# Kernel tuning notes

Measured on AMD Instinct MI355X. Metric: run time of the kernel, lower is better.

## Reference

```python
import jax, jax.numpy as jnp
import numpy as np

HEADS = 8
TOPK = 32
LN_EPS = 1e-5


def _ln(x, g, b):
    m = jnp.mean(x, axis=-1, keepdims=True)
    v = jnp.var(x, axis=-1, keepdims=True)
    return (x - m) * jax.lax.rsqrt(v + LN_EPS) * g + b


def _split_heads(t):
    B, N, I = t.shape
    return t.reshape(B, N, HEADS, I // HEADS).transpose(0, 2, 1, 3)


def _merge_heads(t):
    B, H, N, D = t.shape
    return t.transpose(0, 2, 1, 3).reshape(B, N, H * D)


def _mha(xq, xkv, wq, wk, wv, wo, bo):
    # standard softmax cross-attention (SDPA branch, topk<=0), scale=1/sqrt(d_head)
    q = _split_heads(xq @ wq)
    k = _split_heads(xkv @ wk)
    v = _split_heads(xkv @ wv)
    scale = q.shape[-1] ** -0.5
    attn = jax.nn.softmax(jnp.einsum('bhnd,bhmd->bhnm', q, k) * scale, axis=-1)
    o = jnp.einsum('bhnm,bhmd->bhnd', attn, v)
    return _merge_heads(o) @ wo + bo


def _topk_attn(x, wq, wk, wv, wo, bo):
    # top-k sparse self-attention branch: softmax over the k largest logits per query,
    # all other attention weights are exactly zero -> equivalent to gathering the
    # selected value rows and contracting (avoids materializing the scattered matrix).
    q = _split_heads(x @ wq)
    k = _split_heads(x @ wk)
    v = _split_heads(x @ wv)
    scale = q.shape[-1] ** -0.5
    dots = jnp.einsum('bhnd,bhmd->bhnm', q, k) * scale  # [B,H,N,N]
    top_dots, top_inds = jax.lax.top_k(dots, TOPK)      # [B,H,N,K]
    top_attn = jax.nn.softmax(top_dots, axis=-1)
    # v_sel[b,h,n,k,d] = v[b,h,top_inds[b,h,n,k],d]
    v_sel = jnp.take_along_axis(v[:, :, None, :, :], top_inds[..., None], axis=3)
    o = jnp.einsum('bhnk,bhnkd->bhnd', top_attn, v_sel)
    return _merge_heads(o) @ wo + bo


def _geglu_ff(x, w1, b1, w2, b2):
    h = x @ w1 + b1
    a, g = jnp.split(h, 2, axis=-1)
    return (a * jax.nn.gelu(g, approximate=False)) @ w2 + b2


def _forward(x, context,
             ctx_wq, ctx_wk, ctx_wv, ctx_wo, ctx_bo, cn_g, cn_b,
             im_wq, im_wk, im_wv, im_wo, im_bo,
             xc_wq, xc_wk, xc_wv, xc_wo, xc_bo,
             ffc_w1, ffc_b1, ffc_w2, ffc_b2,
             ffi_w1, ffi_b1, ffi_w2, ffi_b2,
             n1_g, n1_b, n2_g, n2_b, n3_g, n3_b):
    # context self-attention (nx_enhanced=1) + context feed-forward
    cn = _ln(context, cn_g, cn_b)
    c = context + _mha(cn, cn, ctx_wq, ctx_wk, ctx_wv, ctx_wo, ctx_bo)
    c = c + _geglu_ff(c, ffc_w1, ffc_b1, ffc_w2, ffc_b2)
    # image-token top-k sparse self-attention
    h = x + _topk_attn(_ln(x, n1_g, n1_b), im_wq, im_wk, im_wv, im_wo, im_bo)
    # image -> context cross-attention
    h = h + _mha(_ln(h, n2_g, n2_b), c, xc_wq, xc_wk, xc_wv, xc_wo, xc_bo)
    # image feed-forward (GEGLU)
    h = h + _geglu_ff(_ln(h, n3_g, n3_b), ffi_w1, ffi_b1, ffi_w2, ffi_b2)
    return h


def setup_inputs() -> dict:
    key = jax.random.key(0)
    ki = iter(jax.random.split(key, 64))
    def w(*shape):
        return jax.random.normal(next(ki), shape, jnp.float32) * 0.02
    C, D, I = 768, 512, 512
    inp = dict(
        x=jax.random.normal(next(ki), (2, 2304, D), jnp.float32),
        context=jax.random.normal(next(ki), (2, 256, C), jnp.float32),
        spatial_shapes=jnp.array([[48, 48]], dtype=jnp.int32),  # 48*48 == 2304
        ctx_wq=w(C, I), ctx_wk=w(C, I), ctx_wv=w(C, I), ctx_wo=w(I, C),
        ctx_bo=jnp.zeros((C,), jnp.float32),
        cn_g=jnp.ones((C,), jnp.float32), cn_b=jnp.zeros((C,), jnp.float32),
        im_wq=w(D, I), im_wk=w(D, I), im_wv=w(D, I), im_wo=w(I, D),
        im_bo=jnp.zeros((D,), jnp.float32),
        xc_wq=w(D, I), xc_wk=w(C, I), xc_wv=w(C, I), xc_wo=w(I, D),
        xc_bo=jnp.zeros((D,), jnp.float32),
        ffc_w1=w(C, 8 * C), ffc_b1=jnp.zeros((8 * C,), jnp.float32),
        ffc_w2=w(4 * C, C), ffc_b2=jnp.zeros((C,), jnp.float32),
        ffi_w1=w(D, 8 * D), ffi_b1=jnp.zeros((8 * D,), jnp.float32),
        ffi_w2=w(4 * D, D), ffi_b2=jnp.zeros((D,), jnp.float32),
        n1_g=jnp.ones((D,), jnp.float32), n1_b=jnp.zeros((D,), jnp.float32),
        n2_g=jnp.ones((D,), jnp.float32), n2_b=jnp.zeros((D,), jnp.float32),
        n3_g=jnp.ones((D,), jnp.float32), n3_b=jnp.zeros((D,), jnp.float32),
    )
    return inp


def reference(x, context, spatial_shapes,
              ctx_wq, ctx_wk, ctx_wv, ctx_wo, ctx_bo, cn_g, cn_b,
              im_wq, im_wk, im_wv, im_wo, im_bo,
              xc_wq, xc_wk, xc_wv, xc_wo, xc_bo,
              ffc_w1, ffc_b1, ffc_w2, ffc_b2,
              ffi_w1, ffi_b1, ffi_w2, ffi_b2,
              n1_g, n1_b, n2_g, n2_b, n3_g, n3_b):
    del spatial_shapes  # only consumed by the (disabled) deformable path
    return _forward(x, context,
                    ctx_wq, ctx_wk, ctx_wv, ctx_wo, ctx_bo, cn_g, cn_b,
                    im_wq, im_wk, im_wv, im_wo, im_bo,
                    xc_wq, xc_wk, xc_wv, xc_wo, xc_bo,
                    ffc_w1, ffc_b1, ffc_w2, ffc_b2,
                    ffi_w1, ffi_b1, ffi_w2, ffi_b2,
                    n1_g, n1_b, n2_g, n2_b, n3_g, n3_b)
```

## Files before the change

### kernel.cpp

```cpp
#include <hip/hip_runtime.h>
#include <hip/hip_bf16.h>
#include <hip/hip_fp16.h>
#include <cmath>

typedef unsigned short u16;
typedef unsigned long long ull;
typedef __attribute__((ext_vector_type(8))) short short8;
typedef __attribute__((ext_vector_type(4))) float f32x4;
typedef __attribute__((ext_vector_type(4))) unsigned short u16x4;

__device__ __forceinline__ u16 f2bf(float x) {
    unsigned u = __float_as_uint(x);
    u += 0x7fffu + ((u >> 16) & 1u);
    return (u16)(u >> 16);
}
__device__ __forceinline__ float bf2f(u16 b) {
    return __uint_as_float(((unsigned)b) << 16);
}

__device__ __forceinline__ unsigned h2key(unsigned hb) {
    return (hb & 0x8000u) ? (hb ^ 0xFFFFu) : (hb | 0x8000u);
}
__device__ __forceinline__ float key2f(unsigned k) {
    unsigned hb = (k & 0x8000u) ? (k ^ 0x8000u) : (k ^ 0xFFFFu);
    return __half2float(__ushort_as_half((unsigned short)hb));
}

typedef __attribute__((address_space(3))) unsigned int as3_uint;
typedef __attribute__((address_space(1))) unsigned int as1_uint;
__device__ __forceinline__ void gload_lds16(const u16* g, u16* l) {
    __builtin_amdgcn_global_load_lds(
        (as1_uint*)(unsigned long long)(const void*)g,
        (as3_uint*)(unsigned int)(unsigned long long)(const void*)l,
        16, 0, 0);
}

__device__ __forceinline__ float gelu_exact(float g) {
    return 0.5f * g * (1.f + erff(g * 0.70710678118654752f));
}

struct TBatch {
    const float* src[16];
    u16* dst[16];
    int K[16];
    int N[16];
    int start[17];
};

__global__ void k_transpose_cast_batch(TBatch tb) {
    __shared__ float tile[32][33];
    int t = blockIdx.x;
    int m = 0;
    while (t >= tb.start[m + 1]) ++m;
    int rel = t - tb.start[m];
    const int K = tb.K[m], N = tb.N[m];
    const int ntx = N >> 5;
    const int n0 = (rel % ntx) * 32, k0 = (rel / ntx) * 32;
    const float* __restrict__ in = tb.src[m];
    u16* __restrict__ out = tb.dst[m];
    int tx = threadIdx.x, ty = threadIdx.y;
#pragma unroll
    for (int j = 0; j < 4; ++j)
        tile[ty + j * 8][tx] = in[(size_t)(k0 + ty + j * 8) * N + n0 + tx];
    __syncthreads();
#pragma unroll
    for (int j = 0; j < 4; ++j)
        out[(size_t)(n0 + ty + j * 8) * K + k0 + tx] = f2bf(tile[tx][ty + j * 8]);
}

__global__ void k_vtrans16(const u16* __restrict__ in, int stride, int coloff,
                           u16* __restrict__ out) {
    __shared__ int tile[32][33];
    int tx = threadIdx.x, ty = threadIdx.y;
    int d0 = blockIdx.x * 32, k0 = blockIdx.y * 32, b = blockIdx.z;
#pragma unroll
    for (int j = 0; j < 4; ++j)
        tile[ty + j * 8][tx] = in[(size_t)(b * 256 + k0 + ty + j * 8) * stride + coloff + d0 + tx];
    __syncthreads();
#pragma unroll
    for (int j = 0; j < 4; ++j)
        out[(size_t)(b * 512 + d0 + ty + j * 8) * 256 + k0 + tx] = (u16)tile[tx][ty + j * 8];
}

__global__ __launch_bounds__(256)
void k_ln_bf16(const float* __restrict__ in, const float* __restrict__ gam,
               const float* __restrict__ bet, u16* __restrict__ out, int F) {
    int lane = threadIdx.x & 63, w = threadIdx.x >> 6;
    int row = blockIdx.x * 4 + w;
    const int F4 = F >> 2;
    const float4* r4 = reinterpret_cast<const float4*>(in + (size_t)row * F);
    const float4* g4 = reinterpret_cast<const float4*>(gam);
    const float4* b4 = reinterpret_cast<const float4*>(bet);
    float s = 0.f, s2 = 0.f;
    for (int j = lane; j < F4; j += 64) {
        float4 v = r4[j];
        s += v.x + v.y + v.z + v.w;
        s2 += v.x * v.x + v.y * v.y + v.z * v.z + v.w * v.w;
    }
#pragma unroll
    for (int off = 32; off; off >>= 1) { s += __shfl_xor(s, off); s2 += __shfl_xor(s2, off); }
    float mean = s / F;
    float var  = s2 / F - mean * mean;
    float inv  = 1.f / sqrtf(var + 1e-5f);
    u16x4* o4 = reinterpret_cast<u16x4*>(out + (size_t)row * F);
    for (int j = lane; j < F4; j += 64) {
        float4 v = r4[j], gm = g4[j], bt = b4[j];
        u16x4 o;
        o[0] = f2bf((v.x - mean) * inv * gm.x + bt.x);
        o[1] = f2bf((v.y - mean) * inv * gm.y + bt.y);
        o[2] = f2bf((v.z - mean) * inv * gm.z + bt.z);
        o[3] = f2bf((v.w - mean) * inv * gm.w + bt.w);
        o4[j] = o;
    }
}

template <int BM, int BN>
__global__ __launch_bounds__(256)
void gemm_bt(const u16* __restrict__ A, const u16* __restrict__ Bt,
             const float* __restrict__ bias, const float* __restrict__ res,
             float* __restrict__ out32, u16* __restrict__ out16,
             int M, int N, int K) {
    constexpr int WM = BM / 2, WN = BN / 2, FM = WM / 16, FN = WN / 16;
    __shared__ __align__(16) u16 As[BM * 32];
    __shared__ __align__(16) u16 Bs[BN * 32];
    const int tid = threadIdx.x;
    const int lane = tid & 63;
    const int wid = tid >> 6;
    const int wr = wid >> 1, wc = wid & 1;
    const int nwg = gridDim.x * gridDim.y;
    int lin = blockIdx.y * gridDim.x + blockIdx.x;
    lin = (lin & 7) * (nwg >> 3) + (lin >> 3);
    const int m0 = (lin / gridDim.x) * BM, n0 = (lin % gridDim.x) * BN;
    const int r16 = lane & 15;
    const int g8  = (lane >> 4) * 8;
    const int w16 = wid * 16;
    const int ln4 = lane >> 2;
    const int cb8 = (lane & 3) * 8;

    const f32x4 zero4 = {0.f, 0.f, 0.f, 0.f};
    f32x4 acc[FM][FN];
#pragma unroll
    for (int m = 0; m < FM; ++m)
#pragma unroll
        for (int n = 0; n < FN; ++n) acc[m][n] = zero4;

    for (int k0 = 0; k0 < K; k0 += 32) {
#pragma unroll
        for (int p = 0; p < BM / 64; ++p) {
            const int rb = p * 64 + w16;
            gload_lds16(A + (size_t)(m0 + rb + ln4) * K + k0 + cb8, &As[rb * 32]);
        }
#pragma unroll
        for (int p = 0; p < BN / 64; ++p) {
            const int rb = p * 64 + w16;
            gload_lds16(Bt + (size_t)(n0 + rb + ln4) * K + k0 + cb8, &Bs[rb * 32]);
        }
        __syncthreads();
        short8 af[FM], bfr[FN];
#pragma unroll
        for (int m = 0; m < FM; ++m)
            af[m] = *reinterpret_cast<const short8*>(&As[(wr * WM + m * 16 + r16) * 32 + g8]);
#pragma unroll
        for (int n = 0; n < FN; ++n)
            bfr[n] = *reinterpret_cast<const short8*>(&Bs[(wc * WN + n * 16 + r16) * 32 + g8]);
#pragma unroll
        for (int m = 0; m < FM; ++m)
#pragma unroll
            for (int n = 0; n < FN; ++n)
                acc[m][n] = __builtin_amdgcn_mfma_f32_16x16x32_bf16(af[m], bfr[n], acc[m][n], 0, 0, 0);
        __syncthreads();
    }

    const int rg = (lane >> 4) * 4;
#pragma unroll
    for (int m = 0; m < FM; ++m) {
#pragma unroll
        for (int n = 0; n < FN; ++n) {
#pragma unroll
            for (int j = 0; j < 4; ++j) {
                int row = m0 + wr * WM + m * 16 + rg + j;
                int col = n0 + wc * WN + n * 16 + r16;
                float v = acc[m][n][j];
                if (bias) v += bias[col];
                size_t off = (size_t)row * N + col;
                if (res) v += res[off];
                if (out32) out32[off] = v;
                if (out16) out16[off] = f2bf(v);
            }
        }
    }
}

template <int BM>
__global__ __launch_bounds__(256)
void gemm_geglu(const u16* __restrict__ A, const u16* __restrict__ Bt,
                const float* __restrict__ bias, u16* __restrict__ out16,
                int M, int Nh, int K) {
    constexpr int WM = BM / 2, FM = WM / 16;
    __shared__ __align__(16) u16 As[BM * 32];
    __shared__ __align__(16) u16 Bs[128 * 32];
    const int tid = threadIdx.x;
    const int lane = tid & 63;
    const int wid = tid >> 6;
    const int wr = wid >> 1, wc = wid & 1;
    const int nwg = gridDim.x * gridDim.y;
    int lin = blockIdx.y * gridDim.x + blockIdx.x;
    lin = (lin & 7) * (nwg >> 3) + (lin >> 3);
    const int m0 = (lin / gridDim.x) * BM, n0 = (lin % gridDim.x) * 64;
    const int r16 = lane & 15;
    const int g8  = (lane >> 4) * 8;
    const int w16 = wid * 16;
    const int ln4 = lane >> 2;
    const int cb8 = (lane & 3) * 8;

    const f32x4 zero4 = {0.f, 0.f, 0.f, 0.f};
    f32x4 acc_a[FM][2], acc_g[FM][2];
#pragma unroll
    for (int m = 0; m < FM; ++m)
#pragma unroll
        for (int n = 0; n < 2; ++n) { acc_a[m][n] = zero4; acc_g[m][n] = zero4; }

    for (int k0 = 0; k0 < K; k0 += 32) {
#pragma unroll
        for (int p = 0; p < BM / 64; ++p) {
            const int rb = p * 64 + w16;
            gload_lds16(A + (size_t)(m0 + rb + ln4) * K + k0 + cb8, &As[rb * 32]);
        }
        gload_lds16(Bt + (size_t)(n0 + w16 + ln4) * K + k0 + cb8, &Bs[w16 * 32]);
        gload_lds16(Bt + (size_t)(Nh + n0 + w16 + ln4) * K + k0 + cb8, &Bs[(64 + w16) * 32]);
        __syncthreads();
        short8 af[FM], ba[2], bg[2];
#pragma unroll
        for (int m = 0; m < FM; ++m)
            af[m] = *reinterpret_cast<const short8*>(&As[(wr * WM + m * 16 + r16) * 32 + g8]);
#pragma unroll
        for (int n = 0; n < 2; ++n) {
            ba[n] = *reinterpret_cast<const short8*>(&Bs[(wc * 32 + n * 16 + r16) * 32 + g8]);
            bg[n] = *reinterpret_cast<const short8*>(&Bs[(64 + wc * 32 + n * 16 + r16) * 32 + g8]);
        }
#pragma unroll
        for (int m = 0; m < FM; ++m)
#pragma unroll
            for (int n = 0; n < 2; ++n) {
                acc_a[m][n] = __builtin_amdgcn_mfma_f32_16x16x32_bf16(af[m], ba[n], acc_a[m][n], 0, 0, 0);
                acc_g[m][n] = __builtin_amdgcn_mfma_f32_16x16x32_bf16(af[m], bg[n], acc_g[m][n], 0, 0, 0);
            }
        __syncthreads();
    }

    const int rg = (lane >> 4) * 4;
#pragma unroll
    for (int m = 0; m < FM; ++m) {
#pragma unroll
        for (int n = 0; n < 2; ++n) {
#pragma unroll
            for (int j = 0; j < 4; ++j) {
                int row = m0 + wr * WM + m * 16 + rg + j;
                int col = n0 + wc * 32 + n * 16 + r16;
                float a = acc_a[m][n][j] + bias[col];
                float g = acc_g[m][n][j] + bias[Nh + col];
                out16[(size_t)row * Nh + col] = f2bf(a * gelu_exact(g));
            }
        }
    }
}

__global__ __launch_bounds__(256)
void k_attn_mfma(const u16* __restrict__ Qb, int sq, const u16* __restrict__ Kb,
                 int sk, const u16* __restrict__ VT, u16* __restrict__ out, int NQ) {
    __shared__ float sc[16][268];
    __shared__ u16   pb[16][268];
    const int tid = threadIdx.x, lane = tid & 63, w = tid >> 6;
    const int nqb = NQ >> 4;
    const int h = blockIdx.x & 7;
    const int rest = blockIdx.x >> 3;
    const int b = rest / nqb;
    const int q0 = (rest % nqb) << 4;
    const int r16 = lane & 15, g8 = (lane >> 4) * 8, rq = (lane >> 4) * 4;

    const size_t qrow = ((size_t)(b * NQ + q0 + r16)) * sq + h * 64;
    const short8 af0 = *reinterpret_cast<const short8*>(Qb + qrow + g8);
    const short8 af1 = *reinterpret_cast<const short8*>(Qb + qrow + 32 + g8);
    const u16* kb = Kb + (size_t)b * 256 * sk + h * 64;
    const f32x4 zero4 = {0.f, 0.f, 0.f, 0.f};
#pragma unroll
    for (int t = 0; t < 4; ++t) {
        const size_t krow = (size_t)(t * 64 + w * 16 + r16) * sk;
        const short8 bf0 = *reinterpret_cast<const short8*>(kb + krow + g8);
        const short8 bf1 = *reinterpret_cast<const short8*>(kb + krow + 32 + g8);
        f32x4 acc = __builtin_amdgcn_mfma_f32_16x16x32_bf16(af0, bf0, zero4, 0, 0, 0);
        acc = __builtin_amdgcn_mfma_f32_16x16x32_bf16(af1, bf1, acc, 0, 0, 0);
        const int col = t * 64 + w * 16 + r16;
#pragma unroll
        for (int j = 0; j < 4; ++j) sc[rq + j][col] = acc[j] * 0.125f;
    }
    __syncthreads();
#pragma unroll
    for (int qi = 0; qi < 4; ++qi) {
        const int q = w * 4 + qi;
        float4 v = *reinterpret_cast<const float4*>(&sc[q][lane * 4]);
        float m = fmaxf(fmaxf(v.x, v.y), fmaxf(v.z, v.w));
#pragma unroll
        for (int off = 32; off; off >>= 1) m = fmaxf(m, __shfl_xor(m, off));
        float e0 = expf(v.x - m), e1 = expf(v.y - m), e2 = expf(v.z - m), e3 = expf(v.w - m);
        float sum = e0 + e1 + e2 + e3;
#pragma unroll
        for (int off = 32; off; off >>= 1) sum += __shfl_xor(sum, off);
        float inv = 1.f / sum;
        u16x4 p4;
        p4[0] = f2bf(e0 * inv); p4[1] = f2bf(e1 * inv);
        p4[2] = f2bf(e2 * inv); p4[3] = f2bf(e3 * inv);
        *reinterpret_cast<u16x4*>(&pb[q][lane * 4]) = p4;
    }
    __syncthreads();
    f32x4 o = zero4;
    const u16* vt = VT + ((size_t)(b * 512 + h * 64 + w * 16 + r16)) * 256;
#pragma unroll
    for (int kk = 0; kk < 8; ++kk) {
        const short8 pa = *reinterpret_cast<const short8*>(&pb[r16][kk * 32 + g8]);
        const short8 vv = *reinterpret_cast<const short8*>(vt + kk * 32 + g8);
        o = __builtin_amdgcn_mfma_f32_16x16x32_bf16(pa, vv, o, 0, 0, 0);
    }
#pragma unroll
    for (int j = 0; j < 4; ++j)
        out[((size_t)(b * NQ + q0 + rq + j)) * 512 + h * 64 + w * 16 + r16] = f2bf(o[j]);
}

__global__ __launch_bounds__(256)
void gemm_scores(const u16* __restrict__ QKV, u16* __restrict__ keys) {
    __shared__ __align__(16) u16 As[128 * 32];
    __shared__ __align__(16) u16 Bs[128 * 32];
    const int tid = threadIdx.x;
    const int lane = tid & 63;
    const int wid = tid >> 6;
    const int wr = wid >> 1, wc = wid & 1;
    int lin = blockIdx.x;
    lin = (lin & 7) * 648 + (lin >> 3);
    const int bh = lin / 324;
    const int rel = lin % 324;
    const int m0 = (rel / 18) * 128, n0 = (rel % 18) * 128;
    const int b = bh >> 3, h = bh & 7;
    const u16* Qb = QKV + (size_t)b * 2304 * 1536 + h * 64;
    const u16* Kb = Qb + 512;
    const int r16 = lane & 15;
    const int g8  = (lane >> 4) * 8;
    const int w16 = wid * 16;
    const int ln4 = lane >> 2;
    const int cb8 = (lane & 3) * 8;

    const f32x4 zero4 = {0.f, 0.f, 0.f, 0.f};
    f32x4 acc[4][4];
#pragma unroll
    for (int m = 0; m < 4; ++m)
#pragma unroll
        for (int n = 0; n < 4; ++n) acc[m][n] = zero4;

#pragma unroll
    for (int k0 = 0; k0 < 64; k0 += 32) {
#pragma unroll
        for (int p = 0; p < 2; ++p) {
            const int rb = p * 64 + w16;
            gload_lds16(Qb + (size_t)(m0 + rb + ln4) * 1536 + k0 + cb8, &As[rb * 32]);
            gload_lds16(Kb + (size_t)(n0 + rb + ln4) * 1536 + k0 + cb8, &Bs[rb * 32]);
        }
        __syncthreads();
        short8 af[4], bfr[4];
#pragma unroll
        for (int m = 0; m < 4; ++m)
            af[m] = *reinterpret_cast<const short8*>(&As[(wr * 64 + m * 16 + r16) * 32 + g8]);
#pragma unroll
        for (int n = 0; n < 4; ++n)
            bfr[n] = *reinterpret_cast<const short8*>(&Bs[(wc * 64 + n * 16 + r16) * 32 + g8]);
#pragma unroll
        for (int m = 0; m < 4; ++m)
#pragma unroll
            for (int n = 0; n < 4; ++n)
                acc[m][n] = __builtin_amdgcn_mfma_f32_16x16x32_bf16(af[m], bfr[n], acc[m][n], 0, 0, 0);
        __syncthreads();
    }

    u16* kout = keys + (size_t)bh * 2304 * 2304;
    const int rg = (lane >> 4) * 4;
#pragma unroll
    for (int m = 0; m < 4; ++m) {
#pragma unroll
        for (int n = 0; n < 4; ++n) {
#pragma unroll
            for (int j = 0; j < 4; ++j) {
                int row = m0 + wr * 64 + m * 16 + rg + j;
                int col = n0 + wc * 64 + n * 16 + r16;
                unsigned hb = __half_as_ushort(__float2half(acc[m][n][j] * 0.125f));
                kout[(size_t)row * 2304 + col] = (u16)h2key(hb);
            }
        }
    }
}

__global__ __launch_bounds__(256)
void k_topk_sel(const u16* __restrict__ keys, const u16* __restrict__ QKV,
                u16* __restrict__ out) {
    __shared__ int   ilist[4][32];
    __shared__ float wlist[4][32];
    const int tid = threadIdx.x, lane = tid & 63, w = tid >> 6;
    const int h = blockIdx.x & 7;
    const int t7 = blockIdx.x >> 3;
    const int b = t7 / 576;
    const int q = (t7 % 576) * 4 + w;

    const u16* krow = keys + ((size_t)((b * 8 + h) * 2304) + q) * 2304;
    const ull ltm = (1ull << lane) - 1ull;
    unsigned key[36];
    unsigned kmax = 0;
#pragma unroll
    for (int j = 0; j < 36; ++j) {
        key[j] = krow[lane + j * 64];
        kmax = key[j] > kmax ? key[j] : kmax;
    }
#pragma unroll
    for (int off = 32; off; off >>= 1) {
        unsigned o = (unsigned)__shfl_xor((int)kmax, off);
        kmax = o > kmax ? o : kmax;
    }
    unsigned thr = 0;
    for (int bit = 15; bit >= 0; --bit) {
        unsigned cand = thr | (1u << bit);
        int c = 0;
#pragma unroll
        for (int j = 0; j < 36; ++j)
            c += (int)__popcll(__ballot(key[j] >= cand));
        if (c >= 32) { thr = cand; if (c == 32) break; }
    }
    int tot = 0;
#pragma unroll
    for (int j = 0; j < 36; ++j) {
        bool p = key[j] > thr;
        ull m = __ballot(p);
        if (p) {
            int pos = tot + (int)__popcll(m & ltm);
            ilist[w][pos] = j * 64 + lane;
            wlist[w][pos] = key2f(key[j]);
        }
        tot += (int)__popcll(m);
    }
    const int r = 32 - tot;
    const float tv = key2f(thr);
    int t2 = 0;
#pragma unroll
    for (int j = 0; j < 36; ++j) {
        bool p = (key[j] == thr);
        ull m = __ballot(p);
        if (p) {
            int pos = t2 + (int)__popcll(m & ltm);
            if (pos < r) { ilist[w][tot + pos] = j * 64 + lane; wlist[w][tot + pos] = tv; }
        }
        t2 += (int)__popcll(m);
    }
    const float mf = key2f(kmax);
    float e = 0.f;
    if (lane < 32) e = expf(wlist[w][lane] - mf);
    float sum = e;
#pragma unroll
    for (int off = 32; off; off >>= 1) sum += __shfl_xor(sum, off);
    if (lane < 32) wlist[w][lane] = e / sum;
    const u16* vb = QKV + (size_t)b * 2304 * 1536 + 1024 + h * 64 + lane;
    u16 vr[32];
#pragma unroll
    for (int i = 0; i < 32; ++i)
        vr[i] = vb[(size_t)ilist[w][i] * 1536];
    float o = 0.f;
#pragma unroll
    for (int i = 0; i < 32; ++i)
        o += wlist[w][i] * bf2f(vr[i]);
    out[((size_t)(b * 2304 + q)) * 512 + h * 64 + lane] = f2bf(o);
}

static constexpr size_t O_WQKVC = 0;
static constexpr size_t O_WOC   = O_WQKVC + 2359296;
static constexpr size_t O_W1C   = O_WOC + 786432;
static constexpr size_t O_W2C   = O_W1C + 9437184;
static constexpr size_t O_WQKVI = O_W2C + 4718592;
static constexpr size_t O_WOI   = O_WQKVI + 1572864;
static constexpr size_t O_WQX   = O_WOI + 524288;
static constexpr size_t O_WKVX  = O_WQX + 524288;
static constexpr size_t O_WOX   = O_WKVX + 1572864;
static constexpr size_t O_W1I   = O_WOX + 524288;
static constexpr size_t O_W2I   = O_W1I + 4194304;
static constexpr size_t O_CF16  = O_W2I + 2097152;
static constexpr size_t O_H     = O_CF16 + 786432;
static constexpr size_t O_H2    = O_H + 9437184;
static constexpr size_t O_S     = O_H2 + 9437184;
static constexpr size_t O_CN16  = O_S;
static constexpr size_t O_QKVC  = O_CN16 + 786432;
static constexpr size_t O_VTC   = O_QKVC + 1572864;
static constexpr size_t O_AO16  = O_VTC + 524288;
static constexpr size_t O_CBUF  = O_AO16 + 524288;
static constexpr size_t O_C16   = O_CBUF + 1572864;
static constexpr size_t O_AG16  = O_C16 + 786432;
static constexpr size_t O_XLN   = O_S;
static constexpr size_t O_QKVI  = O_XLN + 4718592;
static constexpr size_t O_KEYS  = O_QKVI + 14155776;
static constexpr size_t O_TO16  = O_KEYS + 169869312;
static constexpr size_t O_H2LN  = O_S;
static constexpr size_t O_XQ    = O_H2LN + 4718592;
static constexpr size_t O_KVX   = O_XQ + 4718592;
static constexpr size_t O_VTX   = O_KVX + 1048576;
static constexpr size_t O_XO16  = O_VTX + 524288;
static constexpr size_t O_H3    = O_S;
static constexpr size_t O_AGI   = O_H3 + 4718592;

extern "C" void kernel_launch(void* const* d_in, const int* in_sizes, int n_in,
                              void* d_out, int out_size, void* d_ws, size_t ws_size,
                              hipStream_t stream) {
    (void)in_sizes; (void)n_in; (void)out_size; (void)ws_size;
    const float* x      = (const float*)d_in[0];
    const float* ctx    = (const float*)d_in[1];
    const float* ctx_wq = (const float*)d_in[3];
    const float* ctx_wk = (const float*)d_in[4];
    const float* ctx_wv = (const float*)d_in[5];
    const float* ctx_wo = (const float*)d_in[6];
    const float* ctx_bo = (const float*)d_in[7];
    const float* cn_g   = (const float*)d_in[8];
    const float* cn_b   = (const float*)d_in[9];
    const float* im_wq  = (const float*)d_in[10];
    const float* im_wk  = (const float*)d_in[11];
    const float* im_wv  = (const float*)d_in[12];
    const float* im_wo  = (const float*)d_in[13];
    const float* im_bo  = (const float*)d_in[14];
    const float* xc_wq  = (const float*)d_in[15];
    const float* xc_wk  = (const float*)d_in[16];
    const float* xc_wv  = (const float*)d_in[17];
    const float* xc_wo  = (const float*)d_in[18];
    const float* xc_bo  = (const float*)d_in[19];
    const float* ffc_w1 = (const float*)d_in[20];
    const float* ffc_b1 = (const float*)d_in[21];
    const float* ffc_w2 = (const float*)d_in[22];
    const float* ffc_b2 = (const float*)d_in[23];
    const float* ffi_w1 = (const float*)d_in[24];
    const float* ffi_b1 = (const float*)d_in[25];
    const float* ffi_w2 = (const float*)d_in[26];
    const float* ffi_b2 = (const float*)d_in[27];
    const float* n1_g   = (const float*)d_in[28];
    const float* n1_b   = (const float*)d_in[29];
    const float* n2_g   = (const float*)d_in[30];
    const float* n2_b   = (const float*)d_in[31];
    const float* n3_g   = (const float*)d_in[32];
    const float* n3_b   = (const float*)d_in[33];
    char* ws = (char*)d_ws;
    float* out = (float*)d_out;
    auto Wp = [&](size_t off) { return (u16*)(ws + off); };
    auto Fp = [&](size_t off) { return (float*)(ws + off); };
    dim3 tb(32, 8);

    TBatch tbat;
    const float* srcs[16] = {ctx_wq, ctx_wk, ctx_wv, ctx_wo, ffc_w1, ffc_w2,
                             im_wq, im_wk, im_wv, im_wo, xc_wq, xc_wk, xc_wv,
                             xc_wo, ffi_w1, ffi_w2};
    const size_t dsts[16] = {O_WQKVC, O_WQKVC + 786432, O_WQKVC + 1572864, O_WOC,
                             O_W1C, O_W2C,
                             O_WQKVI, O_WQKVI + 524288, O_WQKVI + 1048576, O_WOI,
                             O_WQX, O_WKVX, O_WKVX + 786432, O_WOX,
                             O_W1I, O_W2I};
    const int Ks[16] = {768, 768, 768, 512, 768, 3072, 512, 512, 512, 512,
                        512, 768, 768, 512, 512, 2048};
    const int Ns[16] = {512, 512, 512, 768, 6144, 768, 512, 512, 512, 512,
                        512, 512, 512, 512, 4096, 512};
    int acc = 0;
    for (int i = 0; i < 16; ++i) {
        tbat.src[i] = srcs[i];
        tbat.dst[i] = Wp(dsts[i]);
        tbat.K[i] = Ks[i];
        tbat.N[i] = Ns[i];
        tbat.start[i] = acc;
        acc += (Ns[i] >> 5) * (Ks[i] >> 5);
    }
    tbat.start[16] = acc;
    k_transpose_cast_batch<<<acc, tb, 0, stream>>>(tbat);

    k_ln_bf16<<<128, 256, 0, stream>>>(ctx, cn_g, cn_b, Wp(O_CN16), 768);
    gemm_bt<64, 64><<<dim3(24, 8), 256, 0, stream>>>(Wp(O_CN16), Wp(O_WQKVC), nullptr, nullptr, nullptr, Wp(O_QKVC), 512, 1536, 768);
    k_vtrans16<<<dim3(16, 8, 2), tb, 0, stream>>>(Wp(O_QKVC), 1536, 1024, Wp(O_VTC));
    k_attn_mfma<<<256, 256, 0, stream>>>(Wp(O_QKVC), 1536, Wp(O_QKVC) + 512, 1536, Wp(O_VTC), Wp(O_AO16), 256);
    gemm_bt<64, 64><<<dim3(12, 8), 256, 0, stream>>>(Wp(O_AO16), Wp(O_WOC), ctx_bo, ctx, Fp(O_CBUF), Wp(O_C16), 512, 768, 512);
    gemm_geglu<128><<<dim3(48, 4), 256, 0, stream>>>(Wp(O_C16), Wp(O_W1C), ffc_b1, Wp(O_AG16), 512, 3072, 768);
    gemm_bt<64, 64><<<dim3(12, 8), 256, 0, stream>>>(Wp(O_AG16), Wp(O_W2C), ffc_b2, Fp(O_CBUF), nullptr, Wp(O_CF16), 512, 768, 3072);

    k_ln_bf16<<<1152, 256, 0, stream>>>(x, n1_g, n1_b, Wp(O_XLN), 512);
    gemm_bt<128, 128><<<dim3(12, 36), 256, 0, stream>>>(Wp(O_XLN), Wp(O_WQKVI), nullptr, nullptr, nullptr, Wp(O_QKVI), 4608, 1536, 512);
    gemm_scores<<<5184, 256, 0, stream>>>(Wp(O_QKVI), Wp(O_KEYS));
    k_topk_sel<<<9216, 256, 0, stream>>>(Wp(O_KEYS), Wp(O_QKVI), Wp(O_TO16));
    gemm_bt<128, 64><<<dim3(8, 36), 256, 0, stream>>>(Wp(O_TO16), Wp(O_WOI), im_bo, x, Fp(O_H), nullptr, 4608, 512, 512);

    k_ln_bf16<<<1152, 256, 0, stream>>>(Fp(O_H), n2_g, n2_b, Wp(O_H2LN), 512);
    gemm_bt<128, 64><<<dim3(8, 36), 256, 0, stream>>>(Wp(O_H2LN), Wp(O_WQX), nullptr, nullptr, nullptr, Wp(O_XQ), 4608, 512, 512);
    gemm_bt<64, 64><<<dim3(16, 8), 256, 0, stream>>>(Wp(O_CF16), Wp(O_WKVX), nullptr, nullptr, nullptr, Wp(O_KVX), 512, 1024, 768);
    k_vtrans16<<<dim3(16, 8, 2), tb, 0, stream>>>(Wp(O_KVX), 1024, 512, Wp(O_VTX));
    k_attn_mfma<<<2304, 256, 0, stream>>>(Wp(O_XQ), 512, Wp(O_KVX), 1024, Wp(O_VTX), Wp(O_XO16), 2304);
    gemm_bt<128, 64><<<dim3(8, 36), 256, 0, stream>>>(Wp(O_XO16), Wp(O_WOX), xc_bo, Fp(O_H), Fp(O_H2), nullptr, 4608, 512, 512);

    k_ln_bf16<<<1152, 256, 0, stream>>>(Fp(O_H2), n3_g, n3_b, Wp(O_H3), 512);
    gemm_geglu<128><<<dim3(32, 36), 256, 0, stream>>>(Wp(O_H3), Wp(O_W1I), ffi_b1, Wp(O_AGI), 4608, 2048, 512);
    gemm_bt<128, 64><<<dim3(8, 36), 256, 0, stream>>>(Wp(O_AGI), Wp(O_W2I), ffi_b2, Fp(O_H2), out, nullptr, 4608, 512, 2048);
}
```

Measured before the change: 498.3 us.

## Prefetch full K in score GEMM and early-exit threshold counting in top-k select

The score GEMM now loads both 32-wide K slices into double-size shared buffers up front and syncs once, removing the per-slice load/sync round trip. The top-k radix threshold search now counts ballots in blocks of six and stops counting once 32 hits are found, and it no longer breaks early on an exact count of 32. The row max is now taken over the 32 selected logits by shuffle rather than over all keys up front. This trades more shared memory and registers in the GEMM, and possibly more bit iterations in the search, for fewer barriers and fewer ballots per iteration.

New measurement: 498.7 us. About the same (+0.1%).

```diff
diff --git a/kernel.cpp b/kernel.cpp
--- a/kernel.cpp
+++ b/kernel.cpp
@@ -328,8 +328,8 @@
 
 __global__ __launch_bounds__(256)
 void gemm_scores(const u16* __restrict__ QKV, u16* __restrict__ keys) {
-    __shared__ __align__(16) u16 As[128 * 32];
-    __shared__ __align__(16) u16 Bs[128 * 32];
+    __shared__ __align__(16) u16 As[2][128 * 32];
+    __shared__ __align__(16) u16 Bs[2][128 * 32];
     const int tid = threadIdx.x;
     const int lane = tid & 63;
     const int wid = tid >> 6;
@@ -348,6 +348,17 @@
     const int ln4 = lane >> 2;
     const int cb8 = (lane & 3) * 8;
 
+#pragma unroll
+    for (int kk = 0; kk < 2; ++kk) {
+#pragma unroll
+        for (int p = 0; p < 2; ++p) {
+            const int rb = p * 64 + w16;
+            gload_lds16(Qb + (size_t)(m0 + rb + ln4) * 1536 + kk * 32 + cb8, &As[kk][rb * 32]);
+            gload_lds16(Kb + (size_t)(n0 + rb + ln4) * 1536 + kk * 32 + cb8, &Bs[kk][rb * 32]);
+        }
+    }
+    __syncthreads();
+
     const f32x4 zero4 = {0.f, 0.f, 0.f, 0.f};
     f32x4 acc[4][4];
 #pragma unroll
@@ -355,29 +366,21 @@
 #pragma unroll
         for (int n = 0; n < 4; ++n) acc[m][n] = zero4;
 
-#pragma unroll
-    for (int k0 = 0; k0 < 64; k0 += 32) {
-#pragma unroll
-        for (int p = 0; p < 2; ++p) {
-            const int rb = p * 64 + w16;
-            gload_lds16(Qb + (size_t)(m0 + rb + ln4) * 1536 + k0 + cb8, &As[rb * 32]);
-            gload_lds16(Kb + (size_t)(n0 + rb + ln4) * 1536 + k0 + cb8, &Bs[rb * 32]);
-        }
-        __syncthreads();
-        short8 af[4], bfr[4];
+    short8 af[2][4], bfr[2][4];
+#pragma unroll
+    for (int kk = 0; kk < 2; ++kk)
+#pragma unroll
+        for (int m = 0; m < 4; ++m) {
+            af[kk][m] = *reinterpret_cast<const short8*>(&As[kk][(wr * 64 + m * 16 + r16) * 32 + g8]);
+            bfr[kk][m] = *reinterpret_cast<const short8*>(&Bs[kk][(wc * 64 + m * 16 + r16) * 32 + g8]);
+        }
+#pragma unroll
+    for (int kk = 0; kk < 2; ++kk)
 #pragma unroll
         for (int m = 0; m < 4; ++m)
-            af[m] = *reinterpret_cast<const short8*>(&As[(wr * 64 + m * 16 + r16) * 32 + g8]);
-#pragma unroll
-        for (int n = 0; n < 4; ++n)
-            bfr[n] = *reinterpret_cast<const short8*>(&Bs[(wc * 64 + n * 16 + r16) * 32 + g8]);
-#pragma unroll
-        for (int m = 0; m < 4; ++m)
 #pragma unroll
             for (int n = 0; n < 4; ++n)
-                acc[m][n] = __builtin_amdgcn_mfma_f32_16x16x32_bf16(af[m], bfr[n], acc[m][n], 0, 0, 0);
-        __syncthreads();
-    }
+                acc[m][n] = __builtin_amdgcn_mfma_f32_16x16x32_bf16(af[kk][m], bfr[kk][n], acc[m][n], 0, 0, 0);
 
     u16* kout = keys + (size_t)bh * 2304 * 2304;
     const int rg = (lane >> 4) * 4;
@@ -410,25 +413,24 @@
     const u16* krow = keys + ((size_t)((b * 8 + h) * 2304) + q) * 2304;
     const ull ltm = (1ull << lane) - 1ull;
     unsigned key[36];
-    unsigned kmax = 0;
-#pragma unroll
-    for (int j = 0; j < 36; ++j) {
+#pragma unroll
+    for (int j = 0; j < 36; ++j)
         key[j] = krow[lane + j * 64];
-        kmax = key[j] > kmax ? key[j] : kmax;
-    }
-#pragma unroll
-    for (int off = 32; off; off >>= 1) {
-        unsigned o = (unsigned)__shfl_xor((int)kmax, off);
-        kmax = o > kmax ? o : kmax;
-    }
+
     unsigned thr = 0;
     for (int bit = 15; bit >= 0; --bit) {
-        unsigned cand = thr | (1u << bit);
-        int c = 0;
-#pragma unroll
-        for (int j = 0; j < 36; ++j)
-            c += (int)__popcll(__ballot(key[j] >= cand));
-        if (c >= 32) { thr = cand; if (c == 32) break; }
+        const unsigned cand = thr | (1u << bit);
+        int c = 0, done = 0;
+#pragma unroll
+        for (int blk = 0; blk < 6; ++blk) {
+            if (!done) {
+#pragma unroll
+                for (int u = 0; u < 6; ++u)
+                    c += (int)__popcll(__ballot(key[blk * 6 + u] >= cand));
+                if (c >= 32) done = 1;
+            }
+        }
+        if (c >= 32) thr = cand;
     }
     int tot = 0;
 #pragma unroll
@@ -455,9 +457,11 @@
         }
         t2 += (int)__popcll(m);
     }
-    const float mf = key2f(kmax);
-    float e = 0.f;
-    if (lane < 32) e = expf(wlist[w][lane] - mf);
+    float wv = (lane < 32) ? wlist[w][lane] : -3.0e38f;
+    float mf = wv;
+#pragma unroll
+    for (int off = 32; off; off >>= 1) mf = fmaxf(mf, __shfl_xor(mf, off));
+    float e = (lane < 32) ? expf(wv - mf) : 0.f;
     float sum = e;
 #pragma unroll
     for (int off = 32; off; off >>= 1) sum += __shfl_xor(sum, off);
```
